# Kernel optimization log

Measured on AMD Instinct MI355X. Metric: run time of the kernel, lower is better.

## Reference

```python
import jax, jax.numpy as jnp
import numpy as np

B, S, E, H = 2, 2048, 2048, 16
D = E // H  # head_dim = 128


def setup_inputs() -> dict:
    key = jax.random.key(0)
    k1, k2, k3, k4, k5 = jax.random.split(key, 5)
    hidden_states = jax.random.normal(k1, (B, S, E), dtype=jnp.float32)
    # causal mask, broadcastable to attn_shape (B, q, H, k)
    causal = jnp.tril(jnp.ones((S, S), dtype=bool))  # [q, k]
    attention_mask = jnp.broadcast_to(causal[None, :, None, :], (B, S, 1, S))
    c_attn_w = jax.random.normal(k2, (E, E + 2 * D), dtype=jnp.float32) * (E ** -0.5)
    c_attn_b = jax.random.normal(k3, (E + 2 * D,), dtype=jnp.float32) * 0.02
    c_proj_w = jax.random.normal(k4, (E, E), dtype=jnp.float32) * (E ** -0.5)
    c_proj_b = jax.random.normal(k5, (E,), dtype=jnp.float32) * 0.02
    return {
        "hidden_states": hidden_states,
        "attention_mask": attention_mask,
        "c_attn_w": c_attn_w,
        "c_attn_b": c_attn_b,
        "c_proj_w": c_proj_w,
        "c_proj_b": c_proj_b,
    }


def reference(hidden_states, attention_mask, c_attn_w, c_attn_b, c_proj_w, c_proj_b):
    b, s, e = hidden_states.shape
    h, d = H, D
    qkv = hidden_states @ c_attn_w + c_attn_b            # [b, s, e + 2d]
    query = qkv[..., :e]                                 # [b, s, e]
    key = qkv[..., e:e + d]                              # [b, s, d] (single shared KV head)
    value = qkv[..., e + d:]                             # [b, s, d]
    scale = 1.0 / (d ** 0.5)                             # scale_attn_weights, unscale=1
    q = query.reshape(b, s * h, d)
    # QK^T with MQA broadcast: [b, s*h, k]
    scores = jnp.einsum('bqd,bkd->bqk', q, key) * scale
    scores = scores.reshape(b, s, h, s)                  # attn_shape (b, q, h, k)
    mask_value = jnp.finfo(scores.dtype).min
    scores = jnp.where(attention_mask, scores, mask_value)
    probs = jax.nn.softmax(scores, axis=-1)              # fp32 softmax (upcast is no-op in fp32)
    attn = jnp.einsum('bqk,bkd->bqd', probs.reshape(b, s * h, s), value)
    attn = attn.reshape(b, s, e)
    return attn @ c_proj_w + c_proj_b
```

## Files before the change

### kernel.cpp

```cpp
#include <hip/hip_runtime.h>
#include <math.h>


typedef __attribute__((ext_vector_type(8))) short short8;
typedef __attribute__((ext_vector_type(8))) __bf16 bf16x8;
typedef __attribute__((ext_vector_type(4))) float floatx4;
typedef __attribute__((ext_vector_type(4))) unsigned short ushort4v;
typedef __attribute__((ext_vector_type(2))) unsigned uint2v;
typedef unsigned short ushort;

__device__ __forceinline__ ushort f2bf(float f) {
    unsigned u = __builtin_bit_cast(unsigned, f);
    u += 0x7fffu + ((u >> 16) & 1u);
    return (ushort)(u >> 16);
}
__device__ __forceinline__ unsigned pk2(float a, float b) {
    return (unsigned)f2bf(a) | ((unsigned)f2bf(b) << 16);
}

template <typename V>
__device__ __forceinline__ auto mfma_try(V a, V b, floatx4 c, int)
    -> decltype(__builtin_amdgcn_mfma_f32_16x16x32_bf16(a, b, c, 0, 0, 0)) {
    return __builtin_amdgcn_mfma_f32_16x16x32_bf16(a, b, c, 0, 0, 0);
}
template <typename V>
__device__ __forceinline__ floatx4 mfma_try(V a, V b, floatx4 c, long) {
    return __builtin_amdgcn_mfma_f32_16x16x32_bf16(
        __builtin_bit_cast(bf16x8, a), __builtin_bit_cast(bf16x8, b), c, 0, 0, 0);
}
__device__ __forceinline__ floatx4 mfma_bf16(short8 a, short8 b, floatx4 c) {
    return mfma_try(a, b, c, 0);
}

__device__ __forceinline__ void gld_lds16(const ushort* g, ushort* l) {
    __builtin_amdgcn_global_load_lds(
        (const __attribute__((address_space(1))) unsigned*)(const void*)g,
        (__attribute__((address_space(3))) unsigned*)(void*)l, 16, 0, 0);
}

__global__ __launch_bounds__(256) void convert_bf16(const float* __restrict__ X,
                                                    ushort* __restrict__ Y, int n4) {
    int i = blockIdx.x * 256 + threadIdx.x;
    if (i >= n4) return;
    float4 v = ((const float4*)X)[i];
    ushort4v o = {f2bf(v.x), f2bf(v.y), f2bf(v.z), f2bf(v.w)};
    *(ushort4v*)&Y[(size_t)i * 4] = o;
}

__global__ __launch_bounds__(256) void transpose_convert(const float* __restrict__ W,
                                                         ushort* __restrict__ WT,
                                                         int K, int N) {
    __shared__ ushort T[64][68];
    const int tid = threadIdx.x;
    const int n0 = blockIdx.x * 64, k0 = blockIdx.y * 64;
    #pragma unroll
    for (int i = 0; i < 4; ++i) {
        int k = (tid >> 4) + i * 16, n = (tid & 15) * 4;
        float4 v = *(const float4*)&W[(size_t)(k0 + k) * N + n0 + n];
        T[n + 0][k] = f2bf(v.x); T[n + 1][k] = f2bf(v.y);
        T[n + 2][k] = f2bf(v.z); T[n + 3][k] = f2bf(v.w);
    }
    __syncthreads();
    #pragma unroll
    for (int i = 0; i < 4; ++i) {
        int idx = tid + i * 256;
        int n = idx >> 4, c4 = idx & 15;
        *(ushort4v*)&WT[(size_t)(n0 + n) * K + k0 + c4 * 4] =
            *(const ushort4v*)&T[n][c4 * 4];
    }
}

__global__ __launch_bounds__(256) void v_transpose(const ushort* __restrict__ qkv,
                                                   ushort* __restrict__ VTg) {
    __shared__ ushort T[64 * 72];
    const int tid = threadIdx.x;
    const int s0 = blockIdx.x * 64, d0 = blockIdx.y * 64, b = blockIdx.z;
    const size_t bS = (size_t)b * 2048;
    #pragma unroll
    for (int i = 0; i < 2; ++i) {
        int idx = tid + i * 256;
        int s = idx >> 3, d8 = idx & 7;
        short8 v = *(const short8*)&qkv[(bS + s0 + s) * 2304 + 2176 + d0 + d8 * 8];
        #pragma unroll
        for (int j = 0; j < 8; ++j)
            T[(d8 * 8 + j) * 72 + s] = (ushort)v[j];
    }
    __syncthreads();
    #pragma unroll
    for (int i = 0; i < 2; ++i) {
        int idx = tid + i * 256;
        int d = idx >> 3, s8 = idx & 7;
        *(short8*)&VTg[((size_t)b * 128 + d0 + d) * 2048 + s0 + s8 * 8] =
            *(const short8*)&T[d * 72 + s8 * 8];
    }
}

#define STAGE_AB(k0_, buf_)                                                    \
    {                                                                          \
        _Pragma("unroll")                                                      \
        for (int i_ = 0; i_ < 4; ++i_) {                                       \
            const int c_ = wid * 4 + i_;                                       \
            const int row_ = c_ * 8 + srow;                                    \
            const int lin_ = sphys ^ ((row_ & 7) << 4);                        \
            gld_lds16(&Ag[(size_t)(m0 + row_) * K + (k0_) + (lin_ >> 1)],      \
                      &As[buf_][c_ * 512]);                                    \
            gld_lds16(&Bg[(size_t)(n0 + row_) * K + (k0_) + (lin_ >> 1)],      \
                      &Bs[buf_][c_ * 512]);                                    \
        }                                                                      \
    }

template <int MODE>
__global__ __launch_bounds__(256, 2) void gemm_db(
    const ushort* __restrict__ Ag, const ushort* __restrict__ Bg,
    const float* __restrict__ bias, void* __restrict__ C, int M, int N, int K)
{
    __shared__ ushort As[2][8192];
    __shared__ ushort Bs[2][8192];
    const int tid = threadIdx.x, lane = tid & 63, wid = tid >> 6;
    const int wr = wid >> 1, wc = wid & 1;
    const int lg = lane >> 4, li = lane & 15;
    const int srow = lane >> 3;
    const int sphys = (lane & 7) * 16;

    const int nbx = gridDim.x;
    const int nwg = nbx * gridDim.y;
    const int bid = blockIdx.y * nbx + blockIdx.x;
    const int swz = (bid & 7) * (nwg >> 3) + (bid >> 3);
    const int m0 = (swz / nbx) * 128, n0 = (swz % nbx) * 128;

    floatx4 acc[4][4] = {};
    const int niter = K >> 6;

    STAGE_AB(0, 0);

    for (int it = 0; it < niter; ++it) {
        __builtin_amdgcn_s_barrier();
        if (it + 1 < niter) {
            STAGE_AB((it + 1) * 64, (it + 1) & 1);
            asm volatile("s_waitcnt vmcnt(8)" ::: "memory");
        } else {
            asm volatile("s_waitcnt vmcnt(0)" ::: "memory");
        }
        __builtin_amdgcn_sched_barrier(0);
        __builtin_amdgcn_s_barrier();
        __builtin_amdgcn_sched_barrier(0);

        const ushort* Ab = As[it & 1];
        const ushort* Bb = Bs[it & 1];
        #pragma unroll
        for (int kk = 0; kk < 2; ++kk) {
            short8 af[4], bfv[4];
            const int pb = (kk * 64 + lg * 16) ^ ((li & 7) << 4);
            #pragma unroll
            for (int m = 0; m < 4; ++m)
                af[m] = *(const short8*)&Ab[(wr * 64 + m * 16 + li) * 64 + (pb >> 1)];
            #pragma unroll
            for (int n = 0; n < 4; ++n)
                bfv[n] = *(const short8*)&Bb[(wc * 64 + n * 16 + li) * 64 + (pb >> 1)];
            #pragma unroll
            for (int m = 0; m < 4; ++m)
                #pragma unroll
                for (int n = 0; n < 4; ++n)
                    acc[m][n] = mfma_bf16(af[m], bfv[n], acc[m][n]);
        }
    }

    #pragma unroll
    for (int m = 0; m < 4; ++m) {
        #pragma unroll
        for (int n = 0; n < 4; ++n) {
            const int col = n0 + wc * 64 + n * 16 + li;
            const float bv = bias[col];
            #pragma unroll
            for (int r = 0; r < 4; ++r) {
                const int row = m0 + wr * 64 + m * 16 + lg * 4 + r;
                float v = acc[m][n][r] + bv;
                if constexpr (MODE == 0) {
                    if (col < 2048) v *= 0.08838834764831845f;
                    ((ushort*)C)[(size_t)row * N + col] = f2bf(v);
                } else {
                    ((float*)C)[(size_t)row * N + col] = v;
                }
            }
        }
    }
}

#define STAGE_KV(t_, Kdst, Vdst)                                               \
    {                                                                          \
        const int k0_ = (t_) * 64;                                             \
        _Pragma("unroll")                                                      \
        for (int i_ = 0; i_ < 4; ++i_) {                                       \
            const int idx_ = gtid + i_ * 256;                                  \
            const int row_ = idx_ >> 4, g_ = idx_ & 15;                        \
            const int src_ = (g_ * 16) ^ ((row_ & 7) << 4);                    \
            gld_lds16(&qkv[(bS + k0_ + row_) * QKV + E + (src_ >> 1)],         \
                      &(Kdst)[(i_ * 256 + gwid * 64) * 8]);                    \
        }                                                                      \
        _Pragma("unroll")                                                      \
        for (int i_ = 0; i_ < 4; ++i_) {                                       \
            const int idx_ = gtid + i_ * 256;                                  \
            const int d_ = idx_ >> 3, kg_ = idx_ & 7;                          \
            gld_lds16(&VTg[((size_t)b * 128 + d_) * 2048 + k0_ +               \
                           ((kg_ ^ (d_ & 7)) << 3)],                           \
                      &(Vdst)[(i_ * 256 + gwid * 64) * 8]);                    \
        }                                                                      \
    }

__global__ __launch_bounds__(512, 2) void attn_kernel(
    const ushort* __restrict__ qkv,
    const ushort* __restrict__ VTg,
    ushort* __restrict__ out)
{
    constexpr int S = 2048, Dh = 128, QKV = 2304, E = 2048;
    __shared__ ushort lds[81920];
    ushort* Ps = lds + 65536;

    const int tid = threadIdx.x, lane = tid & 63, wid = tid >> 6;
    const int gtid = tid & 255;
    const int grp = wid >> 2, gwid = wid & 3;
    const int lg = lane >> 4, li = lane & 15;
    const int pr = blockIdx.x;
    const int h = blockIdx.y, b = blockIdx.z;
    const size_t bS = (size_t)b * S;

    for (int pass = 0; pass < 2; ++pass) {
        const int st = pass ? (15 - pr) : pr;
        const int qA = st * 128 + gwid * 16;
        const int qB = qA + 64;
        const int niter = st + 1;
        const int tbase = grp * niter;

        short8 qfA[4], qfB[4];
        #pragma unroll
        for (int dc = 0; dc < 4; ++dc) {
            qfA[dc] = *(const short8*)&qkv[(bS + qA + li) * QKV + h * Dh + dc * 32 + lg * 8];
            qfB[dc] = *(const short8*)&qkv[(bS + qB + li) * QKV + h * Dh + dc * 32 + lg * 8];
        }

        floatx4 oA[8] = {}, oB[8] = {};
        float mA = -1e30f, lA = 0.f, mB = -1e30f, lB = 0.f;

        STAGE_KV(tbase, lds + (grp * 2) * 8192, lds + 32768 + (grp * 2) * 8192);

        for (int it = 0; it < niter; ++it) {
            const int t = tbase + it;
            __builtin_amdgcn_s_barrier();
            ushort* Kcur = lds + (grp * 2 + (it & 1)) * 8192;
            ushort* Vcur = lds + 32768 + (grp * 2 + (it & 1)) * 8192;
            if (it + 1 < niter) {
                STAGE_KV(t + 1, lds + (grp * 2 + ((it + 1) & 1)) * 8192,
                         lds + 32768 + (grp * 2 + ((it + 1) & 1)) * 8192);
                asm volatile("s_waitcnt vmcnt(8)" ::: "memory");
            } else {
                asm volatile("s_waitcnt vmcnt(0)" ::: "memory");
            }
            __builtin_amdgcn_sched_barrier(0);
            __builtin_amdgcn_s_barrier();

            floatx4 sA[4] = {{0,0,0,0},{0,0,0,0},{0,0,0,0},{0,0,0,0}};
            floatx4 sB[4] = {{0,0,0,0},{0,0,0,0},{0,0,0,0},{0,0,0,0}};
            __builtin_amdgcn_s_setprio(1);
            #pragma unroll
            for (int dc = 0; dc < 4; ++dc) {
                #pragma unroll
                for (int kb = 0; kb < 4; ++kb) {
                    short8 kf = *(const short8*)&Kcur[(kb * 16 + li) * 128 +
                                                      (((dc * 4 + lg) ^ (li & 7)) << 3)];
                    sA[kb] = mfma_bf16(kf, qfA[dc], sA[kb]);
                    sB[kb] = mfma_bf16(kf, qfB[dc], sB[kb]);
                }
            }
            __builtin_amdgcn_s_setprio(0);

            if (t == 2 * st) {
                #pragma unroll
                for (int kb = 0; kb < 4; ++kb)
                    #pragma unroll
                    for (int r = 0; r < 4; ++r)
                        if (kb * 16 + lg * 4 + r > gwid * 16 + li) sA[kb][r] = -2e30f;
            }
            if (t == 2 * st + 1) {
                #pragma unroll
                for (int kb = 0; kb < 4; ++kb)
                    #pragma unroll
                    for (int r = 0; r < 4; ++r) {
                        sA[kb][r] = -2e30f;
                        if (kb * 16 + lg * 4 + r > gwid * 16 + li) sB[kb][r] = -2e30f;
                    }
            }

            {
                float mt = fmaxf(fmaxf(fmaxf(sA[0][0], sA[0][1]), fmaxf(sA[0][2], sA[0][3])),
                                 fmaxf(fmaxf(sA[1][0], sA[1][1]), fmaxf(sA[1][2], sA[1][3])));
                mt = fmaxf(mt, fmaxf(fmaxf(fmaxf(sA[2][0], sA[2][1]), fmaxf(sA[2][2], sA[2][3])),
                                     fmaxf(fmaxf(sA[3][0], sA[3][1]), fmaxf(sA[3][2], sA[3][3]))));
                mt = fmaxf(mt, __shfl_xor(mt, 16));
                mt = fmaxf(mt, __shfl_xor(mt, 32));
                if (!__all(mt <= mA)) {
                    const float mn = fmaxf(mA, mt);
                    const float sc = __expf(mA - mn);
                    mA = mn;
                    lA *= sc;
                    #pragma unroll
                    for (int db = 0; db < 8; ++db) oA[db] *= sc;
                }
                float rs = 0.f;
                #pragma unroll
                for (int kb = 0; kb < 4; ++kb)
                    #pragma unroll
                    for (int r = 0; r < 4; ++r) {
                        float p = __expf(sA[kb][r] - mA);
                        sA[kb][r] = p; rs += p;
                    }
                rs += __shfl_xor(rs, 16);
                rs += __shfl_xor(rs, 32);
                lA += rs;
                #pragma unroll
                for (int kb = 0; kb < 4; ++kb) {
                    const int g = kb * 2 + (lg >> 1);
                    const int sw = ((g ^ (li & 7)) << 3) + ((lg & 1) * 4);
                    uint2v w = {pk2(sA[kb][0], sA[kb][1]), pk2(sA[kb][2], sA[kb][3])};
                    *(uint2v*)&Ps[wid * 2048 + li * 64 + sw] = w;
                }
            }
            {
                float mt = fmaxf(fmaxf(fmaxf(sB[0][0], sB[0][1]), fmaxf(sB[0][2], sB[0][3])),
                                 fmaxf(fmaxf(sB[1][0], sB[1][1]), fmaxf(sB[1][2], sB[1][3])));
                mt = fmaxf(mt, fmaxf(fmaxf(fmaxf(sB[2][0], sB[2][1]), fmaxf(sB[2][2], sB[2][3])),
                                     fmaxf(fmaxf(sB[3][0], sB[3][1]), fmaxf(sB[3][2], sB[3][3]))));
                mt = fmaxf(mt, __shfl_xor(mt, 16));
                mt = fmaxf(mt, __shfl_xor(mt, 32));
                if (!__all(mt <= mB)) {
                    const float mn = fmaxf(mB, mt);
                    const float sc = __expf(mB - mn);
                    mB = mn;
                    lB *= sc;
                    #pragma unroll
                    for (int db = 0; db < 8; ++db) oB[db] *= sc;
                }
                float rs = 0.f;
                #pragma unroll
                for (int kb = 0; kb < 4; ++kb)
                    #pragma unroll
                    for (int r = 0; r < 4; ++r) {
                        float p = __expf(sB[kb][r] - mB);
                        sB[kb][r] = p; rs += p;
                    }
                rs += __shfl_xor(rs, 16);
                rs += __shfl_xor(rs, 32);
                lB += rs;
                #pragma unroll
                for (int kb = 0; kb < 4; ++kb) {
                    const int g = kb * 2 + (lg >> 1);
                    const int sw = ((g ^ (li & 7)) << 3) + ((lg & 1) * 4);
                    uint2v w = {pk2(sB[kb][0], sB[kb][1]), pk2(sB[kb][2], sB[kb][3])};
                    *(uint2v*)&Ps[wid * 2048 + 1024 + li * 64 + sw] = w;
                }
            }

            __builtin_amdgcn_s_setprio(1);
            #pragma unroll
            for (int kc = 0; kc < 2; ++kc) {
                short8 pA = *(const short8*)&Ps[wid * 2048 + li * 64 +
                                                (((kc * 4 + lg) ^ (li & 7)) << 3)];
                short8 pB = *(const short8*)&Ps[wid * 2048 + 1024 + li * 64 +
                                                (((kc * 4 + lg) ^ (li & 7)) << 3)];
                #pragma unroll
                for (int db = 0; db < 8; ++db) {
                    short8 vt = *(const short8*)&Vcur[(db * 16 + li) * 64 +
                                                      (((kc * 4 + lg) ^ (li & 7)) << 3)];
                    oA[db] = mfma_bf16(vt, pA, oA[db]);
                    oB[db] = mfma_bf16(vt, pB, oB[db]);
                }
            }
            __builtin_amdgcn_s_setprio(0);
        }

        float* fbuf = (float*)lds;
        ushort* Pw = lds + wid * 2176;
        __syncthreads();

        if (grp == 1) {
            float* dst = fbuf + (gwid * 64 + lane) * 36;
            #pragma unroll
            for (int db = 0; db < 8; ++db) *(floatx4*)&dst[db * 4] = oA[db];
            dst[32] = mA; dst[33] = lA;
        }
        __syncthreads();
        if (grp == 0) {
            const float* src = fbuf + (gwid * 64 + lane) * 36;
            const float m1 = src[32], l1 = src[33];
            const float mm = fmaxf(mA, m1);
            const float s0 = __expf(mA - mm), s1 = __expf(m1 - mm);
            #pragma unroll
            for (int db = 0; db < 8; ++db) {
                floatx4 o1 = *(const floatx4*)&src[db * 4];
                oA[db] = oA[db] * s0 + o1 * s1;
            }
            lA = lA * s0 + l1 * s1;
        }
        __syncthreads();
        if (grp == 0) {
            const float inv = 1.0f / lA;
            #pragma unroll
            for (int db = 0; db < 8; ++db) {
                *(unsigned*)&Pw[li * 136 + db * 16 + lg * 4]     = pk2(oA[db][0] * inv, oA[db][1] * inv);
                *(unsigned*)&Pw[li * 136 + db * 16 + lg * 4 + 2] = pk2(oA[db][2] * inv, oA[db][3] * inv);
            }
            #pragma unroll
            for (int i = 0; i < 4; ++i) {
                const int q = lane >> 2, d8 = (lane & 3) + i * 4;
                short8 vv = *(const short8*)&Pw[q * 136 + d8 * 8];
                *(short8*)&out[(bS + qA + q) * E + h * Dh + d8 * 8] = vv;
            }
        }
        __syncthreads();

        if (grp == 1) {
            float* dst = fbuf + (gwid * 64 + lane) * 36;
            #pragma unroll
            for (int db = 0; db < 8; ++db) *(floatx4*)&dst[db * 4] = oB[db];
            dst[32] = mB; dst[33] = lB;
        }
        __syncthreads();
        if (grp == 0) {
            const float* src = fbuf + (gwid * 64 + lane) * 36;
            const float m1 = src[32], l1 = src[33];
            const float mm = fmaxf(mB, m1);
            const float s0 = __expf(mB - mm), s1 = __expf(m1 - mm);
            #pragma unroll
            for (int db = 0; db < 8; ++db) {
                floatx4 o1 = *(const floatx4*)&src[db * 4];
                oB[db] = oB[db] * s0 + o1 * s1;
            }
            lB = lB * s0 + l1 * s1;
        }
        __syncthreads();
        if (grp == 0) {
            const float inv = 1.0f / lB;
            #pragma unroll
            for (int db = 0; db < 8; ++db) {
                *(unsigned*)&Pw[li * 136 + db * 16 + lg * 4]     = pk2(oB[db][0] * inv, oB[db][1] * inv);
                *(unsigned*)&Pw[li * 136 + db * 16 + lg * 4 + 2] = pk2(oB[db][2] * inv, oB[db][3] * inv);
            }
            #pragma unroll
            for (int i = 0; i < 4; ++i) {
                const int q = lane >> 2, d8 = (lane & 3) + i * 4;
                short8 vv = *(const short8*)&Pw[q * 136 + d8 * 8];
                *(short8*)&out[(bS + qB + q) * E + h * Dh + d8 * 8] = vv;
            }
        }
        __syncthreads();
    }
}

extern "C" void kernel_launch(void* const* d_in, const int* in_sizes, int n_in,
                              void* d_out, int out_size, void* d_ws, size_t ws_size,
                              hipStream_t stream) {
    (void)in_sizes; (void)n_in; (void)out_size; (void)ws_size;
    const float* hidden   = (const float*)d_in[0];
    const float* c_attn_w = (const float*)d_in[2];
    const float* c_attn_b = (const float*)d_in[3];
    const float* c_proj_w = (const float*)d_in[4];
    const float* c_proj_b = (const float*)d_in[5];
    float* outp = (float*)d_out;

    char* ws = (char*)d_ws;
    ushort* hbf  = (ushort*)ws;
    ushort* W1T  = (ushort*)(ws + (size_t)16777216);
    ushort* W2T  = (ushort*)(ws + (size_t)16777216 + 9437184);
    ushort* qkv  = (ushort*)(ws + (size_t)16777216 + 9437184 + 8388608);
    ushort* VTg  = (ushort*)(ws + (size_t)16777216 + 9437184 + 8388608 + 18874368);
    ushort* attn = hbf;

    convert_bf16<<<8192, 256, 0, stream>>>(hidden, hbf, 4096 * 2048 / 4);
    transpose_convert<<<dim3(36, 32), 256, 0, stream>>>(c_attn_w, W1T, 2048, 2304);
    transpose_convert<<<dim3(32, 32), 256, 0, stream>>>(c_proj_w, W2T, 2048, 2048);

    gemm_db<0><<<dim3(18, 32), 256, 0, stream>>>(hbf, W1T, c_attn_b, qkv, 4096, 2304, 2048);
    v_transpose<<<dim3(32, 2, 2), 256, 0, stream>>>(qkv, VTg);
    attn_kernel<<<dim3(8, 16, 2), 512, 0, stream>>>(qkv, VTg, attn);
    gemm_db<1><<<dim3(16, 32), 256, 0, stream>>>(attn, W2T, c_proj_b, outp, 4096, 2048, 2048);
}
```

Before: 198.0 us.

## Enlarge GEMM tiles to 128x256 with 512-thread eight-wave workgroups

Both projection GEMMs now use 128x256 output tiles computed by 512 threads arranged as 2x4 waves, in place of 128x128 tiles with 256 threads. The staging loads are redistributed over the larger workgroup, and the wait count is adjusted to match the six loads each thread issues per stage. The aim is more operand reuse per LDS load and fewer global reads of the A matrix. In exchange, LDS use per workgroup rises to 96KB and occupancy drops to one workgroup per CU. There are also fewer workgroups, so tail imbalance across CUs can change.

```diff
diff --git a/kernel.cpp b/kernel.cpp
--- a/kernel.cpp
+++ b/kernel.cpp
@@ -95,49 +95,53 @@
     }
 }
 
-#define STAGE_AB(k0_, buf_)                                                    \
+#define STAGE_AB2(k0_, buf_)                                                   \
     {                                                                          \
         _Pragma("unroll")                                                      \
+        for (int i_ = 0; i_ < 2; ++i_) {                                       \
+            const int idx_ = tid + i_ * 512;                      \
+            const int row_ = idx_ >> 3, g_ = idx_ & 7;                         \
+            const int src_ = (g_ * 16) ^ ((row_ & 7) << 4);                    \
+            gld_lds16(&Ag[(size_t)(m0 + row_) * K + (k0_) + (src_ >> 1)],      \
+                      &As[buf_][(i_ * 512 + wid * 64) * 8]);                   \
+        }                                                                      \
+        _Pragma("unroll")                                                      \
         for (int i_ = 0; i_ < 4; ++i_) {                                       \
-            const int c_ = wid * 4 + i_;                                       \
-            const int row_ = c_ * 8 + srow;                                    \
-            const int lin_ = sphys ^ ((row_ & 7) << 4);                        \
-            gld_lds16(&Ag[(size_t)(m0 + row_) * K + (k0_) + (lin_ >> 1)],      \
-                      &As[buf_][c_ * 512]);                                    \
-            gld_lds16(&Bg[(size_t)(n0 + row_) * K + (k0_) + (lin_ >> 1)],      \
-                      &Bs[buf_][c_ * 512]);                                    \
+            const int idx_ = tid + i_ * 512;                      \
+            const int row_ = idx_ >> 3, g_ = idx_ & 7;                         \
+            const int src_ = (g_ * 16) ^ ((row_ & 7) << 4);                    \
+            gld_lds16(&Bg[(size_t)(n0 + row_) * K + (k0_) + (src_ >> 1)],      \
+                      &Bs[buf_][(i_ * 512 + wid * 64) * 8]);                   \
         }                                                                      \
     }
 
 template <int MODE>
-__global__ __launch_bounds__(256, 2) void gemm_db(
+__global__ __launch_bounds__(512, 1) void gemm_big(
     const ushort* __restrict__ Ag, const ushort* __restrict__ Bg,
     const float* __restrict__ bias, void* __restrict__ C, int M, int N, int K)
 {
     __shared__ ushort As[2][8192];
-    __shared__ ushort Bs[2][8192];
+    __shared__ ushort Bs[2][16384];
     const int tid = threadIdx.x, lane = tid & 63, wid = tid >> 6;
-    const int wr = wid >> 1, wc = wid & 1;
+    const int wr = wid >> 2, wc = wid & 3;
     const int lg = lane >> 4, li = lane & 15;
-    const int srow = lane >> 3;
-    const int sphys = (lane & 7) * 16;
 
     const int nbx = gridDim.x;
     const int nwg = nbx * gridDim.y;
     const int bid = blockIdx.y * nbx + blockIdx.x;
     const int swz = (bid & 7) * (nwg >> 3) + (bid >> 3);
-    const int m0 = (swz / nbx) * 128, n0 = (swz % nbx) * 128;
+    const int m0 = (swz / nbx) * 128, n0 = (swz % nbx) * 256;
 
     floatx4 acc[4][4] = {};
     const int niter = K >> 6;
 
-    STAGE_AB(0, 0);
+    STAGE_AB2(0, 0);
 
     for (int it = 0; it < niter; ++it) {
         __builtin_amdgcn_s_barrier();
         if (it + 1 < niter) {
-            STAGE_AB((it + 1) * 64, (it + 1) & 1);
-            asm volatile("s_waitcnt vmcnt(8)" ::: "memory");
+            STAGE_AB2((it + 1) * 64, (it + 1) & 1);
+            asm volatile("s_waitcnt vmcnt(6)" ::: "memory");
         } else {
             asm volatile("s_waitcnt vmcnt(0)" ::: "memory");
         }
@@ -150,13 +154,18 @@
         #pragma unroll
         for (int kk = 0; kk < 2; ++kk) {
             short8 af[4], bfv[4];
-            const int pb = (kk * 64 + lg * 16) ^ ((li & 7) << 4);
-            #pragma unroll
-            for (int m = 0; m < 4; ++m)
-                af[m] = *(const short8*)&Ab[(wr * 64 + m * 16 + li) * 64 + (pb >> 1)];
-            #pragma unroll
-            for (int n = 0; n < 4; ++n)
-                bfv[n] = *(const short8*)&Bb[(wc * 64 + n * 16 + li) * 64 + (pb >> 1)];
+            #pragma unroll
+            for (int m = 0; m < 4; ++m) {
+                const int ra = wr * 64 + m * 16 + li;
+                const int pb = (kk * 64 + lg * 16) ^ ((ra & 7) << 4);
+                af[m] = *(const short8*)&Ab[ra * 64 + (pb >> 1)];
+            }
+            #pragma unroll
+            for (int n = 0; n < 4; ++n) {
+                const int rb = wc * 64 + n * 16 + li;
+                const int pb = (kk * 64 + lg * 16) ^ ((rb & 7) << 4);
+                bfv[n] = *(const short8*)&Bb[rb * 64 + (pb >> 1)];
+            }
             #pragma unroll
             for (int m = 0; m < 4; ++m)
                 #pragma unroll
@@ -478,8 +487,8 @@
     transpose_convert<<<dim3(36, 32), 256, 0, stream>>>(c_attn_w, W1T, 2048, 2304);
     transpose_convert<<<dim3(32, 32), 256, 0, stream>>>(c_proj_w, W2T, 2048, 2048);
 
-    gemm_db<0><<<dim3(18, 32), 256, 0, stream>>>(hbf, W1T, c_attn_b, qkv, 4096, 2304, 2048);
+    gemm_big<0><<<dim3(9, 32), 512, 0, stream>>>(hbf, W1T, c_attn_b, qkv, 4096, 2304, 2048);
     v_transpose<<<dim3(32, 2, 2), 256, 0, stream>>>(qkv, VTg);
     attn_kernel<<<dim3(8, 16, 2), 512, 0, stream>>>(qkv, VTg, attn);
-    gemm_db<1><<<dim3(16, 32), 256, 0, stream>>>(attn, W2T, c_proj_b, outp, 4096, 2048, 2048);
-}
+    gemm_big<1><<<dim3(8, 32), 512, 0, stream>>>(attn, W2T, c_proj_b, outp, 4096, 2048, 2048);
+}
```

After: 221.6 us. +11.9%, slower.
